# Optimization experiments

Hardware: AMD Instinct MI355X
Metric: run time of the kernel (lower is better)

Reference implementation:

```python
import jax, jax.numpy as jnp
import numpy as np

B, H, W, C = 4, 64, 64, 256
D = C // 8  # q/k projection dim


def setup_inputs() -> dict:
    key = jax.random.key(0)
    ks = jax.random.split(key, 5)
    scale = lambda fan_in: 1.0 / np.sqrt(fan_in)
    return {
        "x": jax.random.normal(ks[0], (B, H, W, C), dtype=jnp.float32),
        "wq": jax.random.normal(ks[1], (C, D), dtype=jnp.float32) * scale(C),
        "bq": jnp.zeros((D,), dtype=jnp.float32),
        "wk": jax.random.normal(ks[2], (C, D), dtype=jnp.float32) * scale(C),
        "bk": jnp.zeros((D,), dtype=jnp.float32),
        "wv": jax.random.normal(ks[3], (C, C), dtype=jnp.float32) * scale(C),
        "bv": jnp.zeros((C,), dtype=jnp.float32),
        "wo": jax.random.normal(ks[4], (C, C), dtype=jnp.float32) * scale(C),
        "bo": jnp.zeros((C,), dtype=jnp.float32),
    }


def reference(x, wq, bq, wk, bk, wv, bv, wo, bo):
    b, h, w, c = x.shape
    n = h * w
    xt = x.reshape(b, n, c)  # 1x1 conv == per-pixel linear over channels
    q = xt @ wq + bq                      # [b, n, d]
    k = xt @ wk + bk                      # [b, n, d]
    v = xt @ wv + bv                      # [b, n, c]
    scores = jnp.einsum("bnd,bmd->bnm", q, k) / jnp.sqrt(jnp.float32(k.shape[-1]))
    attn = jax.nn.softmax(scores, axis=-1)  # [b, n, n]
    attended = jnp.einsum("bnm,bmc->bnc", attn, v)  # [b, n, c]
    out = attended @ wo + bo
    return x + out.reshape(b, h, w, c)
```

## Files before the change

### kernel.cpp

```cpp
#include <hip/hip_runtime.h>
#include <math.h>

#define B_   4
#define N_   4096
#define C_   256
#define D_   32

typedef __attribute__((ext_vector_type(8))) short short8;
typedef __attribute__((ext_vector_type(4))) float f32x4;
typedef __attribute__((ext_vector_type(4))) unsigned short us4;
typedef __attribute__((ext_vector_type(4))) unsigned int uint4v;

__device__ __forceinline__ unsigned short f2bf(float f) {
    unsigned int u = __float_as_uint(f);
    u = (u + 0x7FFFu + ((u >> 16) & 1u)) >> 16;
    return (unsigned short)u;
}
__device__ __forceinline__ float bf2f(unsigned short h) {
    return __uint_as_float(((unsigned int)h) << 16);
}
__device__ __forceinline__ unsigned int cvtpk(float a, float b) {
    unsigned int r;
    asm("v_cvt_pk_bf16_f32 %0, %1, %2" : "=v"(r) : "v"(a), "v"(b));
    return r;
}

__device__ __forceinline__ void dma16(const unsigned short* g, unsigned short* l) {
    __builtin_amdgcn_global_load_lds(
        (const __attribute__((address_space(1))) unsigned int*)(uintptr_t)(g),
        (__attribute__((address_space(3))) unsigned int*)(unsigned int)(uintptr_t)(l),
        16, 0, 0);
}

__global__ __launch_bounds__(256) void prep_w_kernel(const float* __restrict__ wq,
                                                     const float* __restrict__ wk,
                                                     const float* __restrict__ wv,
                                                     const float* __restrict__ wo,
                                                     unsigned short* __restrict__ wqkvT,
                                                     unsigned short* __restrict__ woT) {
    int idx = blockIdx.x * 256 + threadIdx.x;
    if (idx < 320 * 256) {
        int n = idx >> 8, c = idx & 255;
        float v = (n < 32) ? wq[c * 32 + n]
                : (n < 64) ? wk[c * 32 + (n - 32)]
                           : wv[c * 256 + (n - 64)];
        wqkvT[idx] = f2bf(v);
    } else {
        int j = idx - 320 * 256;
        int n = j >> 8, c = j & 255;
        woT[j] = f2bf(wo[c * 256 + n]);
    }
}

__global__ __launch_bounds__(256) void qkv_gemm_kernel(const float* __restrict__ x,
        const unsigned short* __restrict__ wqkvT,
        const float* __restrict__ bq, const float* __restrict__ bk, const float* __restrict__ bv,
        unsigned short* __restrict__ qb, unsigned short* __restrict__ kb,
        unsigned short* __restrict__ vT) {
    const int tid = threadIdx.x;
    const int wave = tid >> 6, lane = tid & 63;
    const int quad = lane >> 4, li = lane & 15;
    const int rows0 = blockIdx.x * 32;
    const int bb = rows0 >> 12, ni0 = rows0 & 4095;
    const float kS = 0.17677669529663687f * 1.4426950408889634f;

    __shared__ __align__(16) unsigned short sbuf[10240];

#pragma unroll
    for (int i = 0; i < 8; ++i) {
        int flat = i * 256 + tid;
        int row = flat >> 6, c4 = flat & 63;
        float4 f = *(const float4*)(x + (size_t)(rows0 + row) * 256 + c4 * 4);
        us4 o = { f2bf(f.x), f2bf(f.y), f2bf(f.z), f2bf(f.w) };
        *(us4*)&sbuf[row * 264 + c4 * 4] = o;
    }
    __syncthreads();

    const int rowt = wave & 1;
    const int nt0 = (wave >> 1) * 10;
    const int r0 = rows0 + rowt * 16;

    short8 A[8];
#pragma unroll
    for (int kc = 0; kc < 8; ++kc)
        A[kc] = *(const short8*)&sbuf[(rowt * 16 + li) * 264 + kc * 32 + quad * 8];
    __syncthreads();

#pragma unroll
    for (int j = 0; j < 10; ++j) {
        const int nt = nt0 + j;
        f32x4 acc = {0.f, 0.f, 0.f, 0.f};
#pragma unroll
        for (int kc = 0; kc < 8; ++kc) {
            short8 Bf = *(const short8*)(wqkvT + (size_t)(nt * 16 + li) * 256 + kc * 32 + quad * 8);
            acc = __builtin_amdgcn_mfma_f32_16x16x32_bf16(A[kc], Bf, acc, 0, 0, 0);
        }
        int n = nt * 16 + li;
        float bias = (nt < 2) ? bq[n] : (nt < 4) ? bk[n - 32] : bv[n - 64];
        if (nt < 4) {
            unsigned short* dst = (nt < 2) ? qb : kb;
            float scl = (nt < 2) ? kS : 1.0f;
            int d = (nt < 2) ? n : (n - 32);
#pragma unroll
            for (int jj = 0; jj < 4; ++jj)
                dst[(size_t)(r0 + quad * 4 + jj) * 32 + d] = f2bf((acc[jj] + bias) * scl);
        } else {
            int c = n - 64;
            int lp = rowt * 16 + quad * 4;
            us4 hv = { f2bf(acc[0] + bias), f2bf(acc[1] + bias),
                       f2bf(acc[2] + bias), f2bf(acc[3] + bias) };
            *(us4*)&sbuf[c * 40 + lp] = hv;
        }
    }
    __syncthreads();

    {
        const unsigned short* src = sbuf + tid * 40;
        unsigned short* dstv = vT + ((size_t)(bb * 256 + tid) * 4096 + ni0);
#pragma unroll
        for (int k2 = 0; k2 < 4; ++k2)
            *(short8*)(dstv + k2 * 8) = *(const short8*)(src + k2 * 8);
    }
}

__global__ __launch_bounds__(256, 2) void attn_partial_kernel(
        const unsigned short* __restrict__ qb, const unsigned short* __restrict__ kb,
        const unsigned short* __restrict__ vT,
        unsigned short* __restrict__ Obf, float* __restrict__ ml) {
    const int tid = threadIdx.x;
    const int wave = tid >> 6, lane = tid & 63;
    const int quad = lane >> 4, li = lane & 15;

    const int bid = blockIdx.x;
    const int xcd = bid & 7, jj_ = bid >> 3;
    const int qt = jj_ & 31;
    const int g = (xcd << 1) | (jj_ >> 5);
    const int by = g >> 2, sg = g & 3;
    const int pw = qt * 128 + wave * 32;
    const int key0 = sg * 1024;

    __shared__ __align__(16) unsigned short smem[16896];
    unsigned short* v0 = smem;
    unsigned short* v1 = smem + 8192;

    short8 a_q[2];
#pragma unroll
    for (int qf = 0; qf < 2; ++qf)
        a_q[qf] = *(const short8*)(qb + (size_t)(by * N_ + pw + qf * 16 + li) * 32 + quad * 8);

    const int o8 = lane >> 3, s8 = lane & 7;
    const int sp = s8 ^ o8;
    const int chl = sp >> 2, chk = sp & 3;
    auto stage = [&](int kt, unsigned short* buf) {
#pragma unroll
        for (int h = 0; h < 4; ++h) {
            int ch = ((h * 32 + wave * 8 + o8) << 1) + chl;
            const unsigned short* g2 = vT + (size_t)(by * 256 + ch) * 4096
                                         + key0 + kt * 32 + chk * 8;
            dma16(g2, buf + (h * 256 + wave * 64) * 8);
        }
    };

    stage(0, v0);

    const f32x4 Z = {0.f, 0.f, 0.f, 0.f};
    f32x4 O[2][16];
#pragma unroll
    for (int qf = 0; qf < 2; ++qf)
#pragma unroll
        for (int ct = 0; ct < 16; ++ct) O[qf][ct] = Z;
    f32x4 lsum[2] = {Z, Z};
    short8 ones;
#pragma unroll
    for (int j = 0; j < 8; ++j) ones[j] = (short)0x3F80;

    const int kli = li + (li & 8);
    short8 kf0, kf1;
    {
        const unsigned short* krow = kb + (size_t)(by * N_ + key0) * 32;
        kf0 = *(const short8*)(krow + kli * 32 + quad * 8);
        kf1 = *(const short8*)(krow + (kli + 8) * 32 + quad * 8);
    }

    const int voff = (li >> 1) * 64 + ((((li & 1) * 4 + quad) ^ ((li >> 1) & 7)) * 8);
    const bool oddq = (quad & 1) != 0;

    unsigned short* vc = v0;
    unsigned short* vn = v1;
#pragma unroll 1
    for (int kt = 0; kt < 32; ++kt) {
        __builtin_amdgcn_s_waitcnt(0x0f70);
        __syncthreads();

        short8 kn0 = kf0, kn1 = kf1;
        if (kt < 31) {
            stage(kt + 1, vn);
            const unsigned short* krow = kb + (size_t)(by * N_ + key0 + (kt + 1) * 32) * 32;
            kn0 = *(const short8*)(krow + kli * 32 + quad * 8);
            kn1 = *(const short8*)(krow + (kli + 8) * 32 + quad * 8);
        }

        short8 ap[2];
#pragma unroll
        for (int qf = 0; qf < 2; ++qf) {
            f32x4 s0 = __builtin_amdgcn_mfma_f32_16x16x32_bf16(kf0, a_q[qf], Z, 0, 0, 0);
            f32x4 s1 = __builtin_amdgcn_mfma_f32_16x16x32_bf16(kf1, a_q[qf], Z, 0, 0, 0);
            unsigned int u0 = cvtpk(__builtin_amdgcn_exp2f(s0[0]), __builtin_amdgcn_exp2f(s0[1]));
            unsigned int u1 = cvtpk(__builtin_amdgcn_exp2f(s0[2]), __builtin_amdgcn_exp2f(s0[3]));
            unsigned int vv0 = cvtpk(__builtin_amdgcn_exp2f(s1[0]), __builtin_amdgcn_exp2f(s1[1]));
            unsigned int vv1 = cvtpk(__builtin_amdgcn_exp2f(s1[2]), __builtin_amdgcn_exp2f(s1[3]));
            unsigned int u0x  = (unsigned int)__shfl_xor((int)u0, 16);
            unsigned int u1x  = (unsigned int)__shfl_xor((int)u1, 16);
            unsigned int vv0x = (unsigned int)__shfl_xor((int)vv0, 16);
            unsigned int vv1x = (unsigned int)__shfl_xor((int)vv1, 16);
            uint4v w;
            w.x = oddq ? vv0x : u0;
            w.y = oddq ? vv1x : u1;
            w.z = oddq ? vv0  : u0x;
            w.w = oddq ? vv1  : u1x;
            ap[qf] = *(short8*)&w;
        }

        lsum[0] = __builtin_amdgcn_mfma_f32_16x16x32_bf16(ap[0], ones, lsum[0], 0, 0, 0);
        lsum[1] = __builtin_amdgcn_mfma_f32_16x16x32_bf16(ap[1], ones, lsum[1], 0, 0, 0);
#pragma unroll
        for (int ct = 0; ct < 16; ++ct) {
            short8 bv8 = *(const short8*)(vc + ct * 512 + voff);
            O[0][ct] = __builtin_amdgcn_mfma_f32_16x16x32_bf16(ap[0], bv8, O[0][ct], 0, 0, 0);
            O[1][ct] = __builtin_amdgcn_mfma_f32_16x16x32_bf16(ap[1], bv8, O[1][ct], 0, 0, 0);
        }

        kf0 = kn0; kf1 = kn1;
        unsigned short* t = vc; vc = vn; vn = t;
    }

    __syncthreads();
    unsigned short* att = smem + wave * 4224;
    const int srow = lane & 15, scc = (lane >> 4) * 64;
#pragma unroll
    for (int qf = 0; qf < 2; ++qf) {
#pragma unroll
        for (int ct = 0; ct < 16; ++ct)
#pragma unroll
            for (int r = 0; r < 4; ++r)
                att[(quad * 4 + r) * 264 + ct * 16 + li] = f2bf(O[qf][ct][r]);
        const int pbase = by * N_ + pw + qf * 16;
        unsigned short* dst = Obf + ((size_t)(pbase + srow) * 4 + sg) * 256 + scc;
#pragma unroll
        for (int h = 0; h < 8; ++h)
            *(short8*)(dst + h * 8) = *(const short8*)(att + srow * 264 + scc + h * 8);
        if (li == 0) {
#pragma unroll
            for (int r = 0; r < 4; ++r) {
                int pp = pbase + quad * 4 + r;
                ml[pp * 4 + sg] = lsum[qf][r];
            }
        }
    }
}

__global__ __launch_bounds__(256) void merge_proj_kernel(
        const unsigned short* __restrict__ Obf, const float* __restrict__ ml,
        const unsigned short* __restrict__ woT, const float* __restrict__ x,
        const float* __restrict__ bo, float* __restrict__ out) {
    const int tid = threadIdx.x;
    const int px = blockIdx.x * 16;
    __shared__ __align__(16) unsigned short att[16 * 264];

    {
        const int row = tid >> 4, chc = tid & 15;
        const int p = px + row;
        float lt = ml[p * 4] + ml[p * 4 + 1] + ml[p * 4 + 2] + ml[p * 4 + 3];
        float inv = 1.0f / lt;
        float acc[16];
#pragma unroll
        for (int i = 0; i < 16; ++i) acc[i] = 0.f;
#pragma unroll
        for (int s = 0; s < 4; ++s) {
            const unsigned short* src = Obf + (size_t)(p * 4 + s) * 256 + chc * 16;
            short8 v0 = *(const short8*)(src);
            short8 v1 = *(const short8*)(src + 8);
#pragma unroll
            for (int jj = 0; jj < 8; ++jj) {
                acc[jj]     += bf2f((unsigned short)v0[jj]);
                acc[8 + jj] += bf2f((unsigned short)v1[jj]);
            }
        }
        short8 o0, o1;
#pragma unroll
        for (int jj = 0; jj < 8; ++jj) {
            o0[jj] = (short)f2bf(acc[jj] * inv);
            o1[jj] = (short)f2bf(acc[8 + jj] * inv);
        }
        *(short8*)&att[row * 264 + chc * 16]     = o0;
        *(short8*)&att[row * 264 + chc * 16 + 8] = o1;
    }
    __syncthreads();

    const int wave = tid >> 6, lane = tid & 63;
    const int quad = lane >> 4, li = lane & 15;
    short8 bfr[8];
#pragma unroll
    for (int kc = 0; kc < 8; ++kc)
        bfr[kc] = *(const short8*)&att[li * 264 + kc * 32 + quad * 8];
#pragma unroll
    for (int mt = 0; mt < 4; ++mt) {
        const int mtg = wave * 4 + mt;
        f32x4 acc = {0.f, 0.f, 0.f, 0.f};
#pragma unroll
        for (int kc = 0; kc < 8; ++kc) {
            short8 aw = *(const short8*)(woT + (size_t)(mtg * 16 + li) * 256 + kc * 32 + quad * 8);
            acc = __builtin_amdgcn_mfma_f32_16x16x32_bf16(aw, bfr[kc], acc, 0, 0, 0);
        }
        const int pg = px + li;
        const float4 xv  = *(const float4*)(x  + (size_t)pg * 256 + mtg * 16 + quad * 4);
        const float4 bv4 = *(const float4*)(bo + mtg * 16 + quad * 4);
        float4 o4;
        o4.x = acc[0] + xv.x + bv4.x;
        o4.y = acc[1] + xv.y + bv4.y;
        o4.z = acc[2] + xv.z + bv4.z;
        o4.w = acc[3] + xv.w + bv4.w;
        *(float4*)(out + (size_t)pg * 256 + mtg * 16 + quad * 4) = o4;
    }
}

extern "C" void kernel_launch(void* const* d_in, const int* in_sizes, int n_in,
                              void* d_out, int out_size, void* d_ws, size_t ws_size,
                              hipStream_t stream) {
    const float* x  = (const float*)d_in[0];
    const float* wq = (const float*)d_in[1];
    const float* bq = (const float*)d_in[2];
    const float* wk = (const float*)d_in[3];
    const float* bk = (const float*)d_in[4];
    const float* wv = (const float*)d_in[5];
    const float* bv = (const float*)d_in[6];
    const float* wo = (const float*)d_in[7];
    const float* bo = (const float*)d_in[8];
    float* out = (float*)d_out;

    char* ws = (char*)d_ws;
    unsigned short* wqkvT = (unsigned short*)(ws);
    unsigned short* woT   = (unsigned short*)(ws +   163840);
    unsigned short* qb    = (unsigned short*)(ws +   294912);
    unsigned short* kb    = (unsigned short*)(ws +  1343488);
    unsigned short* vT    = (unsigned short*)(ws +  2392064);
    unsigned short* Obf   = (unsigned short*)(ws + 10780672);
    float*          ml    = (float*)         (ws + 44335104);

    hipLaunchKernelGGL(prep_w_kernel,      dim3(576),  dim3(256), 0, stream, wq, wk, wv, wo, wqkvT, woT);
    hipLaunchKernelGGL(qkv_gemm_kernel,    dim3(512),  dim3(256), 0, stream, x, wqkvT, bq, bk, bv, qb, kb, vT);
    hipLaunchKernelGGL(attn_partial_kernel,dim3(512),  dim3(256), 0, stream, qb, kb, vT, Obf, ml);
    hipLaunchKernelGGL(merge_proj_kernel,  dim3(1024), dim3(256), 0, stream, Obf, ml, woT, x, bo, out);
}
```

Before: 175.0 us.

## Halve queries per wave in attention kernel to double occupancy and grid

Each wave in the attention partial kernel now handles 16 query rows instead of 32, so the block covers 64 queries and the grid doubles to 1024 blocks. Launch bounds rise to 4 blocks per CU, and the halved accumulator state frees registers for that. The aim is more waves to hide latency and better balance across CUs. The cost is that every V tile staged in shared memory is reused by half as many MFMAs, so V and K traffic per query doubles.

```diff
diff --git a/kernel.cpp b/kernel.cpp
--- a/kernel.cpp
+++ b/kernel.cpp
@@ -123,7 +123,7 @@
     }
 }
 
-__global__ __launch_bounds__(256, 2) void attn_partial_kernel(
+__global__ __launch_bounds__(256, 4) void attn_partial_kernel(
         const unsigned short* __restrict__ qb, const unsigned short* __restrict__ kb,
         const unsigned short* __restrict__ vT,
         unsigned short* __restrict__ Obf, float* __restrict__ ml) {
@@ -133,20 +133,17 @@
 
     const int bid = blockIdx.x;
     const int xcd = bid & 7, jj_ = bid >> 3;
-    const int qt = jj_ & 31;
-    const int g = (xcd << 1) | (jj_ >> 5);
+    const int qt = jj_ & 63;
+    const int g = (xcd << 1) | (jj_ >> 6);
     const int by = g >> 2, sg = g & 3;
-    const int pw = qt * 128 + wave * 32;
+    const int pw = qt * 64 + wave * 16;
     const int key0 = sg * 1024;
 
     __shared__ __align__(16) unsigned short smem[16896];
     unsigned short* v0 = smem;
     unsigned short* v1 = smem + 8192;
 
-    short8 a_q[2];
-#pragma unroll
-    for (int qf = 0; qf < 2; ++qf)
-        a_q[qf] = *(const short8*)(qb + (size_t)(by * N_ + pw + qf * 16 + li) * 32 + quad * 8);
+    short8 a_q = *(const short8*)(qb + (size_t)(by * N_ + pw + li) * 32 + quad * 8);
 
     const int o8 = lane >> 3, s8 = lane & 7;
     const int sp = s8 ^ o8;
@@ -164,12 +161,10 @@
     stage(0, v0);
 
     const f32x4 Z = {0.f, 0.f, 0.f, 0.f};
-    f32x4 O[2][16];
-#pragma unroll
-    for (int qf = 0; qf < 2; ++qf)
-#pragma unroll
-        for (int ct = 0; ct < 16; ++ct) O[qf][ct] = Z;
-    f32x4 lsum[2] = {Z, Z};
+    f32x4 O[16];
+#pragma unroll
+    for (int ct = 0; ct < 16; ++ct) O[ct] = Z;
+    f32x4 lsum = Z;
     short8 ones;
 #pragma unroll
     for (int j = 0; j < 8; ++j) ones[j] = (short)0x3F80;
@@ -200,11 +195,10 @@
             kn1 = *(const short8*)(krow + (kli + 8) * 32 + quad * 8);
         }
 
-        short8 ap[2];
-#pragma unroll
-        for (int qf = 0; qf < 2; ++qf) {
-            f32x4 s0 = __builtin_amdgcn_mfma_f32_16x16x32_bf16(kf0, a_q[qf], Z, 0, 0, 0);
-            f32x4 s1 = __builtin_amdgcn_mfma_f32_16x16x32_bf16(kf1, a_q[qf], Z, 0, 0, 0);
+        short8 ap;
+        {
+            f32x4 s0 = __builtin_amdgcn_mfma_f32_16x16x32_bf16(kf0, a_q, Z, 0, 0, 0);
+            f32x4 s1 = __builtin_amdgcn_mfma_f32_16x16x32_bf16(kf1, a_q, Z, 0, 0, 0);
             unsigned int u0 = cvtpk(__builtin_amdgcn_exp2f(s0[0]), __builtin_amdgcn_exp2f(s0[1]));
             unsigned int u1 = cvtpk(__builtin_amdgcn_exp2f(s0[2]), __builtin_amdgcn_exp2f(s0[3]));
             unsigned int vv0 = cvtpk(__builtin_amdgcn_exp2f(s1[0]), __builtin_amdgcn_exp2f(s1[1]));
@@ -218,16 +212,14 @@
             w.y = oddq ? vv1x : u1;
             w.z = oddq ? vv0  : u0x;
             w.w = oddq ? vv1  : u1x;
-            ap[qf] = *(short8*)&w;
-        }
-
-        lsum[0] = __builtin_amdgcn_mfma_f32_16x16x32_bf16(ap[0], ones, lsum[0], 0, 0, 0);
-        lsum[1] = __builtin_amdgcn_mfma_f32_16x16x32_bf16(ap[1], ones, lsum[1], 0, 0, 0);
+            ap = *(short8*)&w;
+        }
+
+        lsum = __builtin_amdgcn_mfma_f32_16x16x32_bf16(ap, ones, lsum, 0, 0, 0);
 #pragma unroll
         for (int ct = 0; ct < 16; ++ct) {
             short8 bv8 = *(const short8*)(vc + ct * 512 + voff);
-            O[0][ct] = __builtin_amdgcn_mfma_f32_16x16x32_bf16(ap[0], bv8, O[0][ct], 0, 0, 0);
-            O[1][ct] = __builtin_amdgcn_mfma_f32_16x16x32_bf16(ap[1], bv8, O[1][ct], 0, 0, 0);
+            O[ct] = __builtin_amdgcn_mfma_f32_16x16x32_bf16(ap, bv8, O[ct], 0, 0, 0);
         }
 
         kf0 = kn0; kf1 = kn1;
@@ -238,23 +230,22 @@
     unsigned short* att = smem + wave * 4224;
     const int srow = lane & 15, scc = (lane >> 4) * 64;
 #pragma unroll
-    for (int qf = 0; qf < 2; ++qf) {
-#pragma unroll
-        for (int ct = 0; ct < 16; ++ct)
-#pragma unroll
-            for (int r = 0; r < 4; ++r)
-                att[(quad * 4 + r) * 264 + ct * 16 + li] = f2bf(O[qf][ct][r]);
-        const int pbase = by * N_ + pw + qf * 16;
+    for (int ct = 0; ct < 16; ++ct)
+#pragma unroll
+        for (int r = 0; r < 4; ++r)
+            att[(quad * 4 + r) * 264 + ct * 16 + li] = f2bf(O[ct][r]);
+    const int pbase = by * N_ + pw;
+    {
         unsigned short* dst = Obf + ((size_t)(pbase + srow) * 4 + sg) * 256 + scc;
 #pragma unroll
         for (int h = 0; h < 8; ++h)
             *(short8*)(dst + h * 8) = *(const short8*)(att + srow * 264 + scc + h * 8);
-        if (li == 0) {
-#pragma unroll
-            for (int r = 0; r < 4; ++r) {
-                int pp = pbase + quad * 4 + r;
-                ml[pp * 4 + sg] = lsum[qf][r];
-            }
+    }
+    if (li == 0) {
+#pragma unroll
+        for (int r = 0; r < 4; ++r) {
+            int pp = pbase + quad * 4 + r;
+            ml[pp * 4 + sg] = lsum[r];
         }
     }
 }
@@ -349,6 +340,6 @@
 
     hipLaunchKernelGGL(prep_w_kernel,      dim3(576),  dim3(256), 0, stream, wq, wk, wv, wo, wqkvT, woT);
     hipLaunchKernelGGL(qkv_gemm_kernel,    dim3(512),  dim3(256), 0, stream, x, wqkvT, bq, bk, bv, qb, kb, vT);
-    hipLaunchKernelGGL(attn_partial_kernel,dim3(512),  dim3(256), 0, stream, qb, kb, vT, Obf, ml);
+    hipLaunchKernelGGL(attn_partial_kernel,dim3(1024), dim3(256), 0, stream, qb, kb, vT, Obf, ml);
     hipLaunchKernelGGL(merge_proj_kernel,  dim3(1024), dim3(256), 0, stream, Obf, ml, woT, x, bo, out);
 }
```

Measured after the change: 186.6 us. 1.07x slower.
